# Kernel optimization log

Hardware: AMD Instinct MI355X
Metric: run time of the kernel (lower is better)

## Reference

```python
import jax, jax.numpy as jnp
import numpy as np

B, L, Z, G = 512, 2713, 58, 8  # batch, chem features, seq len (zeta), d_model (gamma)
H, HD, FF, NL = 8, 1, 2048, 6  # heads, head_dim, ffn dim, layers
RNA_IN, LIN1, LIN2 = 1018, 256, 64
CAT, C1, C2 = LIN2 + Z * G, 64, 8  # 528, 64, 8


def setup_inputs() -> dict:
    key = jax.random.key(0)
    ks = iter(jax.random.split(key, 40))
    r = lambda shape, s=0.05: (jax.random.normal(next(ks), shape, dtype=jnp.float32) * s)
    inp = {
        'rna': jax.random.normal(next(ks), (B, RNA_IN), dtype=jnp.float32),
        'drug': jax.random.normal(next(ks), (B, L, Z), dtype=jnp.float32),
        'lin1_w': r((LIN1, RNA_IN)), 'lin1_b': r((LIN1,)),
        'lin2_w': r((LIN2, LIN1)), 'lin2_b': r((LIN2,)),
        'chem_w': r((G, L)),  # chem_embedding: Linear(2713->8, no bias)
        'pos_w': r((G, Z)),   # pos_embedding on one-hot == its weight columns
        'qkv_w': r((NL, 3 * G, G)), 'qkv_b': r((NL, 3 * G)),
        'out_w': r((NL, G, G)), 'out_b': r((NL, G)),
        'ln1_g': jnp.ones((NL, G), jnp.float32), 'ln1_b': jnp.zeros((NL, G), jnp.float32),
        'ff1_w': r((NL, FF, G)), 'ff1_b': r((NL, FF)),
        'ff2_w': r((NL, G, FF)), 'ff2_b': r((NL, G)),
        'ln2_g': jnp.ones((NL, G), jnp.float32), 'ln2_b': jnp.zeros((NL, G), jnp.float32),
        'c1_w': r((C1, CAT)), 'c1_b': r((C1,)),
        'c2_w': r((C2, C1)), 'c2_b': r((C2,)),
        'c3_w': r((1, C2)), 'c3_b': r((1,)),
    }
    return inp


def _layernorm(x, g, b, eps=1e-5):
    mu = jnp.mean(x, axis=-1, keepdims=True)
    var = jnp.mean(jnp.square(x - mu), axis=-1, keepdims=True)
    return (x - mu) * jax.lax.rsqrt(var + eps) * g + b


def _forward(rna, drug, lin1_w, lin1_b, lin2_w, lin2_b, chem_w, pos_w,
             qkv_w, qkv_b, out_w, out_b, ln1_g, ln1_b,
             ff1_w, ff1_b, ff2_w, ff2_b, ln2_g, ln2_b,
             c1_w, c1_b, c2_w, c2_b, c3_w, c3_b):
    # rna branch: two linear layers (no activation in original forward)
    r = rna @ lin1_w.T + lin1_b
    r = r @ lin2_w.T + lin2_b  # [B, 64]

    # Embedding: E = W_chem @ M + W_pos (the double loop, vectorized)
    E = jnp.einsum('gl,blz->bgz', chem_w, drug) + pos_w[None]  # [B, G, Z]
    x = jnp.transpose(E, (0, 2, 1))  # [B, Z, G] (batch_first transformer input)

    scale = 1.0 / np.sqrt(HD)
    for i in range(NL):  # 6 post-norm TransformerEncoderLayers, relu FFN
        qkv = x @ qkv_w[i].T + qkv_b[i]  # [B, Z, 3G]
        q, k, v = jnp.split(qkv, 3, axis=-1)
        qh = q.reshape(B, Z, H, HD)
        kh = k.reshape(B, Z, H, HD)
        vh = v.reshape(B, Z, H, HD)
        scores = jnp.einsum('bshd,bthd->bhst', qh, kh) * scale
        a = jax.nn.softmax(scores, axis=-1)
        o = jnp.einsum('bhst,bthd->bshd', a, vh).reshape(B, Z, G)
        o = o @ out_w[i].T + out_b[i]
        x = _layernorm(x + o, ln1_g[i], ln1_b[i])
        ff = jax.nn.relu(x @ ff1_w[i].T + ff1_b[i]) @ ff2_w[i].T + ff2_b[i]
        x = _layernorm(x + ff, ln2_g[i], ln2_b[i])

    flat = x.reshape(B, Z * G)  # [B, 464]
    h = jnp.concatenate([r, flat], axis=1)  # [B, 528]
    h = h @ c1_w.T + c1_b
    h = h @ c2_w.T + c2_b
    return h @ c3_w.T + c3_b  # [B, 1]


def reference(rna, drug, lin1_w, lin1_b, lin2_w, lin2_b, chem_w, pos_w,
              qkv_w, qkv_b, out_w, out_b, ln1_g, ln1_b,
              ff1_w, ff1_b, ff2_w, ff2_b, ln2_g, ln2_b,
              c1_w, c1_b, c2_w, c2_b, c3_w, c3_b):
    return _forward(rna, drug, lin1_w, lin1_b, lin2_w, lin2_b, chem_w, pos_w,
                    qkv_w, qkv_b, out_w, out_b, ln1_g, ln1_b,
                    ff1_w, ff1_b, ff2_w, ff2_b, ln2_g, ln2_b,
                    c1_w, c1_b, c2_w, c2_b, c3_w, c3_b)
```

## Files before the change

kernel.cpp:

```cpp
#include <hip/hip_runtime.h>

#define BB 512
#define LDIM 2713
#define ZDIM 58
#define GDIM 8
#define NLAYER 6
#define FFDIM 2048
#define RNAIN 1018
#define CATDIM 528
#define NCAT 1482
#define LQ 679

typedef float v2f __attribute__((ext_vector_type(2)));
typedef float f32x4 __attribute__((ext_vector_type(4)));
typedef _Float16 f16x4 __attribute__((ext_vector_type(4)));

#define OFF_TMATT  0
#define OFF_BR     16384
#define OFF_WCATT  16448
#define OFF_BPRIME 111296
#define OFF_W1H    111360
#define OFF_A2H    160512
#define OFF_EPART  209664

__global__ __launch_bounds__(512, 8) void embed_kernel(
    const float* __restrict__ drug, const float* __restrict__ chem_w,
    float* __restrict__ epart) {
    __shared__ float cwl[LQ * 8 + 8];
    __shared__ float part[8][ZDIM][8];
    const int bq = blockIdx.x;
    const int b = bq >> 2, q = bq & 3;
    const int t = threadIdx.x;
    const int w = t >> 6;
    const int lane = t & 63;
    const int l0 = q * LQ;
    const int nrows = (LDIM - l0 < LQ) ? (LDIM - l0) : LQ;

    #pragma unroll
    for (int g = 0; g < 8; ++g)
        for (int i = t; i < nrows; i += 512)
            cwl[i * 8 + g] = chem_w[g * LDIM + l0 + i];
    __syncthreads();

    {
        int z = (lane < ZDIM) ? lane : (ZDIM - 1);
        const float* dp = drug + (size_t)b * (LDIM * ZDIM) + (size_t)l0 * ZDIM;
        v2f a0 = {0.f, 0.f}, a1 = {0.f, 0.f}, a2 = {0.f, 0.f}, a3 = {0.f, 0.f};
        int r0 = w * 85;
        int r1 = (r0 + 85 < nrows) ? (r0 + 85) : nrows;
        int r = r0;
        for (; r + 4 <= r1; r += 4) {
            float d0 = dp[(r + 0) * ZDIM + z];
            float d1 = dp[(r + 1) * ZDIM + z];
            float d2 = dp[(r + 2) * ZDIM + z];
            float d3 = dp[(r + 3) * ZDIM + z];
            const v2f* c0 = (const v2f*)(cwl + (r + 0) * 8);
            const v2f* c1 = (const v2f*)(cwl + (r + 1) * 8);
            const v2f* c2 = (const v2f*)(cwl + (r + 2) * 8);
            const v2f* c3 = (const v2f*)(cwl + (r + 3) * 8);
            v2f dd;
            dd = (v2f){d0, d0};
            a0 += c0[0] * dd; a1 += c0[1] * dd; a2 += c0[2] * dd; a3 += c0[3] * dd;
            dd = (v2f){d1, d1};
            a0 += c1[0] * dd; a1 += c1[1] * dd; a2 += c1[2] * dd; a3 += c1[3] * dd;
            dd = (v2f){d2, d2};
            a0 += c2[0] * dd; a1 += c2[1] * dd; a2 += c2[2] * dd; a3 += c2[3] * dd;
            dd = (v2f){d3, d3};
            a0 += c3[0] * dd; a1 += c3[1] * dd; a2 += c3[2] * dd; a3 += c3[3] * dd;
        }
        for (; r < r1; ++r) {
            float d = dp[r * ZDIM + z];
            const v2f* cc = (const v2f*)(cwl + r * 8);
            v2f dd = {d, d};
            a0 += cc[0] * dd; a1 += cc[1] * dd; a2 += cc[2] * dd; a3 += cc[3] * dd;
        }
        if (lane < ZDIM) {
            v2f* pr = (v2f*)(&part[w][z][0]);
            pr[0] = a0; pr[1] = a1; pr[2] = a2; pr[3] = a3;
        }
    }
    __syncthreads();
    if (t < 464) {
        int z = t >> 3, g = t & 7;
        float s = 0.f;
        #pragma unroll
        for (int ww = 0; ww < 8; ++ww) s += part[ww][z][g];
        epart[(size_t)bq * 464 + t] = s;
    }
}

__global__ void prep0_kernel(const float* __restrict__ ff1_w, const float* __restrict__ ff2_w,
                             const float* __restrict__ c1_w, const float* __restrict__ lin2_w,
                             const float* __restrict__ lin1_b, const float* __restrict__ lin2_b,
                             float* __restrict__ ws) {
    int tid = blockIdx.x * 256 + threadIdx.x;
    float* TmatT = ws + OFF_TMATT;
    float* bR    = ws + OFF_BR;
    _Float16* w1hp = (_Float16*)(ws + OFF_W1H);
    _Float16* a2hp = (_Float16*)(ws + OFF_A2H);

    int r1 = tid;
    if (r1 < NLAYER * 128 * 32) {
        int li = r1 / 4096, rem = r1 % 4096;
        int ft = rem >> 5, l32 = rem & 31;
        int q = l32 >> 4, i = l32 & 15;
        const float* src = ff1_w + ((size_t)li * FFDIM + ft * 16 + i) * 8 + q * 4;
        size_t dst = ((size_t)(li * 128 + ft) * 32 + l32) * 4;
        #pragma unroll
        for (int j = 0; j < 4; ++j) w1hp[dst + j] = (_Float16)src[j];
        return;
    }
    int r2 = r1 - NLAYER * 128 * 32;
    if (r2 < NLAYER * 128 * 32) {
        int li = r2 / 4096, rem = r2 % 4096;
        int ft = rem >> 5, s = rem & 31;
        int q = s >> 3, i2 = s & 7;
        const float* src = ff2_w + ((size_t)li * GDIM + i2) * FFDIM + ft * 16 + q * 4;
        size_t dst = ((size_t)(li * 128 + ft) * 32 + s) * 4;
        #pragma unroll
        for (int j = 0; j < 4; ++j) a2hp[dst + j] = (_Float16)src[j];
        return;
    }
    int r3 = r2 - NLAYER * 128 * 32;
    if (r3 < 256 * 64) {
        int n = r3 >> 6, j = r3 & 63;
        float a = 0.f;
        for (int m = 0; m < 64; ++m) a += c1_w[j * CATDIM + m] * lin2_w[m * 256 + n];
        TmatT[r3] = a;
        return;
    }
    int r4 = r3 - 256 * 64;
    if (r4 < 64) {
        float a = lin2_b[r4];
        for (int n = 0; n < 256; ++n) a += lin2_w[r4 * 256 + n] * lin1_b[n];
        bR[r4] = a;
    }
}

__global__ void prep1_kernel(const float* __restrict__ lin1_w, const float* __restrict__ c1_w,
                             const float* __restrict__ c1_b, float* __restrict__ ws) {
    int tid = blockIdx.x * 256 + threadIdx.x;
    const float* TmatT = ws + OFF_TMATT;
    const float* bR    = ws + OFF_BR;
    float* WcatT  = ws + OFF_WCATT;
    float* bprime = ws + OFF_BPRIME;
    if (tid < RNAIN * 64) {
        int k = tid >> 6, j = tid & 63;
        float a = 0.f;
        #pragma unroll 4
        for (int n = 0; n < 256; ++n) a += TmatT[n * 64 + j] * lin1_w[n * RNAIN + k];
        WcatT[tid] = a;
        return;
    }
    int q = tid - RNAIN * 64;
    if (q < 464 * 64) {
        int kk = q >> 6, j = q & 63;
        WcatT[(RNAIN + kk) * 64 + j] = c1_w[j * CATDIM + 64 + kk];
        return;
    }
    int j = q - 464 * 64;
    if (j < 64) {
        float a = c1_b[j];
        for (int m = 0; m < 64; ++m) a += c1_w[j * CATDIM + m] * bR[m];
        bprime[j] = a;
    }
}

__global__ __launch_bounds__(1024, 8) void main_kernel(
    const float* __restrict__ epart, const float* __restrict__ pos_w,
    const _Float16* __restrict__ w1h, const _Float16* __restrict__ a2h,
    const float* __restrict__ ff1_b,
    const float* __restrict__ qkv_w, const float* __restrict__ qkv_b,
    const float* __restrict__ out_w, const float* __restrict__ out_b,
    const float* __restrict__ ln1_g, const float* __restrict__ ln1_b,
    const float* __restrict__ ff2_b,
    const float* __restrict__ ln2_g, const float* __restrict__ ln2_b,
    const float* __restrict__ rna, const float* __restrict__ WcatT,
    const float* __restrict__ bprime,
    const float* __restrict__ c2_w, const float* __restrict__ c2_b,
    const float* __restrict__ c3_w, const float* __restrict__ c3_b,
    float* __restrict__ out) {
    __shared__ float smem[12712];
    float* xs    = smem;
    float* qs    = smem + 512;
    float* ks    = smem + 992;
    float* vs    = smem + 1472;
    float* os    = smem + 1952;
    float* part  = smem + 2464;
    float* qkvws = smem + 10656;
    float* qkvbs = smem + 11808;
    float* outws = smem + 11952;
    float* outbs = smem + 12336;
    float* l1gs  = smem + 12384;
    float* l1bs  = smem + 12432;
    float* l2gs  = smem + 12480;
    float* l2bs  = smem + 12528;
    float* f2bs  = smem + 12576;
    float* h1s   = smem + 12624;
    float* h2s   = smem + 12688;

    const int b = blockIdx.x;
    const int t = threadIdx.x;
    const int w = __builtin_amdgcn_readfirstlane(t >> 6);
    const int lane = t & 63;
    const int quad = lane >> 4;
    const int i16 = lane & 15;

    for (int i = t; i < 1152; i += 1024) qkvws[i] = qkv_w[i];
    if (t < 144) qkvbs[t] = qkv_b[t];
    if (t < 384) outws[t] = out_w[t];
    if (t < 48) {
        outbs[t] = out_b[t];
        l1gs[t] = ln1_g[t]; l1bs[t] = ln1_b[t];
        l2gs[t] = ln2_g[t]; l2bs[t] = ln2_b[t];
        f2bs[t] = ff2_b[t];
    }

    if (t < 512) {
        if (t < 464) {
            int z = t >> 3, g = t & 7;
            const float* ep = epart + (size_t)(b * 4) * 464 + t;
            float s = ep[0] + ep[464] + ep[928] + ep[1392] + pos_w[g * ZDIM + z];
            xs[t] = s;
        } else {
            xs[t] = 0.f;
        }
    }
    __syncthreads();

    for (int li = 0; li < NLAYER; ++li) {
        if (t < 464) {
            int z = t >> 3, h = t & 7;
            const float4* xr = (const float4*)(xs + z * 8);
            float4 x0 = xr[0], x1 = xr[1];
            #pragma unroll
            for (int p = 0; p < 3; ++p) {
                int j = p * 8 + h;
                const float4* wr = (const float4*)(qkvws + li * 192 + j * 8);
                float4 w0 = wr[0], w1 = wr[1];
                float a = qkvbs[li * 24 + j]
                        + x0.x * w0.x + x0.y * w0.y + x0.z * w0.z + x0.w * w0.w
                        + x1.x * w1.x + x1.y * w1.y + x1.z * w1.z + x1.w * w1.w;
                float* dst = (p == 0) ? qs : (p == 1) ? ks : vs;
                dst[h * 60 + z] = a;
            }
        }
        __syncthreads();

        if (t < 464) {
            int h = t & 7, s = t >> 3;
            float q = qs[h * 60 + s];
            const float4* kr = (const float4*)(ks + h * 60);
            const float4* vr = (const float4*)(vs + h * 60);
            float sum = 0.f, oa = 0.f;
            #pragma unroll 2
            for (int c = 0; c < 14; ++c) {
                float4 k4 = kr[c], v4 = vr[c];
                float e0 = __expf(q * k4.x); sum += e0; oa += e0 * v4.x;
                float e1 = __expf(q * k4.y); sum += e1; oa += e1 * v4.y;
                float e2 = __expf(q * k4.z); sum += e2; oa += e2 * v4.z;
                float e3 = __expf(q * k4.w); sum += e3; oa += e3 * v4.w;
            }
            {
                const float* kk = ks + h * 60;
                const float* vv = vs + h * 60;
                float e0 = __expf(q * kk[56]); sum += e0; oa += e0 * vv[56];
                float e1 = __expf(q * kk[57]); sum += e1; oa += e1 * vv[57];
            }
            os[t] = oa / sum;
        }
        __syncthreads();

        if (t < 464) {
            int z = t >> 3, g = t & 7;
            const float4* orow = (const float4*)(os + z * 8);
            float4 o0 = orow[0], o1 = orow[1];
            const float4* wr = (const float4*)(outws + li * 64 + g * 8);
            float4 w0 = wr[0], w1 = wr[1];
            float a = outbs[li * 8 + g] + xs[t]
                    + o0.x * w0.x + o0.y * w0.y + o0.z * w0.z + o0.w * w0.w
                    + o1.x * w1.x + o1.y * w1.y + o1.z * w1.z + o1.w * w1.w;
            float s8 = a + __shfl_xor(a, 1);
            s8 += __shfl_xor(s8, 2);
            s8 += __shfl_xor(s8, 4);
            float mu = s8 * 0.125f;
            float d = a - mu;
            float vv = d * d;
            vv += __shfl_xor(vv, 1); vv += __shfl_xor(vv, 2); vv += __shfl_xor(vv, 4);
            float inv = rsqrtf(vv * 0.125f + 1e-5f);
            xs[t] = d * inv * l1gs[li * 8 + g] + l1bs[li * 8 + g];
        }
        __syncthreads();

        {
            f16x4 xb[4];
            #pragma unroll
            for (int nt = 0; nt < 4; ++nt) {
                if (quad < 2) {
                    const float4* xp = (const float4*)(xs + (nt * 16 + i16) * 8 + quad * 4);
                    float4 xv = *xp;
                    xb[nt][0] = (_Float16)xv.x; xb[nt][1] = (_Float16)xv.y;
                    xb[nt][2] = (_Float16)xv.z; xb[nt][3] = (_Float16)xv.w;
                } else {
                    xb[nt][0] = (_Float16)0.f; xb[nt][1] = (_Float16)0.f;
                    xb[nt][2] = (_Float16)0.f; xb[nt][3] = (_Float16)0.f;
                }
            }
            f32x4 oacc[4];
            #pragma unroll
            for (int nt = 0; nt < 4; ++nt) { oacc[nt][0]=0.f; oacc[nt][1]=0.f; oacc[nt][2]=0.f; oacc[nt][3]=0.f; }

            const _Float16* w1p = w1h + ((size_t)(li * 128 + w * 8) * 32) * 4;
            const _Float16* a2p = a2h + ((size_t)(li * 128 + w * 8) * 32) * 4;
            const float* b1p = ff1_b + li * FFDIM + w * 128;

            #pragma unroll 2
            for (int ft = 0; ft < 8; ++ft) {
                f16x4 w1f = {};
                if (lane < 32) w1f = *(const f16x4*)(w1p + (size_t)(ft * 32 + lane) * 4);
                f16x4 a2f = {};
                if (i16 < 8) a2f = *(const f16x4*)(a2p + (size_t)(ft * 32 + quad * 8 + i16) * 4);
                f32x4 b1v = *(const f32x4*)(b1p + ft * 16 + quad * 4);
                #pragma unroll
                for (int nt = 0; nt < 4; ++nt) {
                    f32x4 h = b1v;
                    h = __builtin_amdgcn_mfma_f32_16x16x16f16(w1f, xb[nt], h, 0, 0, 0);
                    h[0] = fmaxf(h[0], 0.f); h[1] = fmaxf(h[1], 0.f);
                    h[2] = fmaxf(h[2], 0.f); h[3] = fmaxf(h[3], 0.f);
                    f16x4 hb;
                    hb[0] = (_Float16)h[0]; hb[1] = (_Float16)h[1];
                    hb[2] = (_Float16)h[2]; hb[3] = (_Float16)h[3];
                    oacc[nt] = __builtin_amdgcn_mfma_f32_16x16x16f16(a2f, hb, oacc[nt], 0, 0, 0);
                }
            }
            if (quad < 2) {
                #pragma unroll
                for (int nt = 0; nt < 4; ++nt) {
                    float4 o4 = make_float4(oacc[nt][0], oacc[nt][1], oacc[nt][2], oacc[nt][3]);
                    *(float4*)(part + ((w * 64 + nt * 16 + i16) * 8 + quad * 4)) = o4;
                }
            }
        }
        __syncthreads();

        if (t < 464) {
            int z = t >> 3, g = t & 7;
            float s = 0.f;
            #pragma unroll
            for (int ww = 0; ww < 16; ++ww) s += part[(ww * 64 + z) * 8 + g];
            float a = xs[t] + s + f2bs[li * 8 + g];
            float s8 = a + __shfl_xor(a, 1);
            s8 += __shfl_xor(s8, 2);
            s8 += __shfl_xor(s8, 4);
            float mu = s8 * 0.125f;
            float d = a - mu;
            float vv = d * d;
            vv += __shfl_xor(vv, 1); vv += __shfl_xor(vv, 2); vv += __shfl_xor(vv, 4);
            float inv = rsqrtf(vv * 0.125f + 1e-5f);
            xs[t] = d * inv * l2gs[li * 8 + g] + l2bs[li * 8 + g];
        }
        __syncthreads();
    }

    {
        float* cat = part;
        float* partial = part + 4096;
        const float* rg = rna + (size_t)b * RNAIN;
        for (int i = t; i < RNAIN; i += 1024) cat[i] = rg[i];
        __syncthreads();
        int j = lane;
        int k0 = w * 93;
        int k1 = (k0 + 93 < NCAT) ? (k0 + 93) : NCAT;
        float a = (w == 0) ? bprime[j] : 0.f;
        #pragma unroll 4
        for (int k = k0; k < k1; ++k) {
            float ck = (k < RNAIN) ? cat[k] : xs[k - RNAIN];
            a += ck * WcatT[k * 64 + j];
        }
        partial[w * 64 + j] = a;
        __syncthreads();
        if (t < 64) {
            float s = 0.f;
            #pragma unroll
            for (int ww = 0; ww < 16; ++ww) s += partial[ww * 64 + t];
            h1s[t] = s;
        }
    }
    __syncthreads();
    if (t < 8) {
        float a2 = c2_b[t];
        #pragma unroll 8
        for (int m = 0; m < 64; ++m) a2 += h1s[m] * c2_w[t * 64 + m];
        h2s[t] = a2;
    }
    __syncthreads();
    if (t == 0) {
        float a3 = c3_b[0];
        #pragma unroll
        for (int jj = 0; jj < 8; ++jj) a3 += h2s[jj] * c3_w[jj];
        out[b] = a3;
    }
}

extern "C" void kernel_launch(void* const* d_in, const int* in_sizes, int n_in,
                              void* d_out, int out_size, void* d_ws, size_t ws_size,
                              hipStream_t stream) {
    const float* rna    = (const float*)d_in[0];
    const float* drug   = (const float*)d_in[1];
    const float* lin1_w = (const float*)d_in[2];
    const float* lin1_b = (const float*)d_in[3];
    const float* lin2_w = (const float*)d_in[4];
    const float* lin2_b = (const float*)d_in[5];
    const float* chem_w = (const float*)d_in[6];
    const float* pos_w  = (const float*)d_in[7];
    const float* qkv_w  = (const float*)d_in[8];
    const float* qkv_b  = (const float*)d_in[9];
    const float* out_w  = (const float*)d_in[10];
    const float* out_b  = (const float*)d_in[11];
    const float* ln1_g  = (const float*)d_in[12];
    const float* ln1_b  = (const float*)d_in[13];
    const float* ff1_w  = (const float*)d_in[14];
    const float* ff1_b  = (const float*)d_in[15];
    const float* ff2_w  = (const float*)d_in[16];
    const float* ff2_b  = (const float*)d_in[17];
    const float* ln2_g  = (const float*)d_in[18];
    const float* ln2_b  = (const float*)d_in[19];
    const float* c1_w   = (const float*)d_in[20];
    const float* c1_b   = (const float*)d_in[21];
    const float* c2_w   = (const float*)d_in[22];
    const float* c2_b   = (const float*)d_in[23];
    const float* c3_w   = (const float*)d_in[24];
    const float* c3_b   = (const float*)d_in[25];
    float* ws  = (float*)d_ws;
    float* out = (float*)d_out;

    float* epart          = ws + OFF_EPART;
    const _Float16* w1h   = (const _Float16*)(ws + OFF_W1H);
    const _Float16* a2h   = (const _Float16*)(ws + OFF_A2H);
    const float* WcatT    = ws + OFF_WCATT;
    const float* bprime   = ws + OFF_BPRIME;

    hipLaunchKernelGGL(embed_kernel, dim3(BB * 4), dim3(512), 0, stream,
                       drug, chem_w, epart);
    hipLaunchKernelGGL(prep0_kernel, dim3(257), dim3(256), 0, stream,
                       ff1_w, ff2_w, c1_w, lin2_w, lin1_b, lin2_b, ws);
    hipLaunchKernelGGL(prep1_kernel, dim3(371), dim3(256), 0, stream,
                       lin1_w, c1_w, c1_b, ws);
    hipLaunchKernelGGL(main_kernel, dim3(BB), dim3(1024), 0, stream,
                       epart, pos_w, w1h, a2h, ff1_b,
                       qkv_w, qkv_b, out_w, out_b,
                       ln1_g, ln1_b, ff2_b, ln2_g, ln2_b,
                       rna, WcatT, bprime, c2_w, c2_b, c3_w, c3_b, out);
}
```

Baseline: 610.7 us.

## Fuse embedding into main kernel and merge prep kernels, drop fp16 weight repack

Moves the chem embedding reduction into the main per-batch kernel, so each 1024-thread block streams its own drug slice in four chunks and skips the epart round trip through global memory. The two prep kernels become one 17-block kernel that keeps the intermediate c1·lin2 product in shared memory. The FFN weights are now read as fp32 from the original layout and converted to fp16 in registers, which removes the repack pass but doubles weight bytes per load and adds conversion work. The embedding now runs on only 512 blocks instead of 2048, so it has less parallelism for the memory-bound drug read, and each prep block recomputes the 256x64 product.

Result: slower. 732.6 us (+20.0%).

```diff
diff --git a/kernel.cpp b/kernel.cpp
--- a/kernel.cpp
+++ b/kernel.cpp
@@ -15,160 +15,63 @@
 typedef float f32x4 __attribute__((ext_vector_type(4)));
 typedef _Float16 f16x4 __attribute__((ext_vector_type(4)));
 
-#define OFF_TMATT  0
-#define OFF_BR     16384
-#define OFF_WCATT  16448
-#define OFF_BPRIME 111296
-#define OFF_W1H    111360
-#define OFF_A2H    160512
-#define OFF_EPART  209664
-
-__global__ __launch_bounds__(512, 8) void embed_kernel(
+#define OFF_WCATT  0
+#define OFF_BPRIME 94848
+
+__global__ __launch_bounds__(1024) void prep_kernel(
+    const float* __restrict__ lin1_w, const float* __restrict__ lin1_b,
+    const float* __restrict__ lin2_w, const float* __restrict__ lin2_b,
+    const float* __restrict__ c1_w, const float* __restrict__ c1_b,
+    float* __restrict__ ws) {
+    __shared__ float Tm[16384];
+    const int t = threadIdx.x;
+    float* WcatT = ws + OFF_WCATT;
+
+    if (blockIdx.x == 16) {
+        if (t < 64) {
+            float a = lin2_b[t];
+            #pragma unroll 4
+            for (int n = 0; n < 256; ++n) a += lin2_w[t * 256 + n] * lin1_b[n];
+            Tm[t] = a;
+        }
+        __syncthreads();
+        if (t < 64) {
+            float a = c1_b[t];
+            #pragma unroll 4
+            for (int m = 0; m < 64; ++m) a += c1_w[t * CATDIM + m] * Tm[m];
+            ws[OFF_BPRIME + t] = a;
+        }
+        for (int i = t; i < 464 * 64; i += 1024) {
+            int kk = i >> 6, j = i & 63;
+            WcatT[(RNAIN + kk) * 64 + j] = c1_w[j * CATDIM + 64 + kk];
+        }
+        return;
+    }
+
+    for (int i = t; i < 16384; i += 1024) {
+        int n = i >> 6, j = i & 63;
+        float a = 0.f;
+        #pragma unroll 8
+        for (int m = 0; m < 64; ++m) a += c1_w[j * CATDIM + m] * lin2_w[m * 256 + n];
+        Tm[i] = a;
+    }
+    __syncthreads();
+    const int k0 = blockIdx.x * 64;
+    const int j = t & 63;
+    for (int kr = t >> 6; kr < 64; kr += 16) {
+        int k = k0 + kr;
+        if (k >= RNAIN) break;
+        float a = 0.f;
+        #pragma unroll 8
+        for (int n = 0; n < 256; ++n) a += Tm[n * 64 + j] * lin1_w[n * RNAIN + k];
+        WcatT[k * 64 + j] = a;
+    }
+}
+
+__global__ __launch_bounds__(1024, 8) void mega_kernel(
     const float* __restrict__ drug, const float* __restrict__ chem_w,
-    float* __restrict__ epart) {
-    __shared__ float cwl[LQ * 8 + 8];
-    __shared__ float part[8][ZDIM][8];
-    const int bq = blockIdx.x;
-    const int b = bq >> 2, q = bq & 3;
-    const int t = threadIdx.x;
-    const int w = t >> 6;
-    const int lane = t & 63;
-    const int l0 = q * LQ;
-    const int nrows = (LDIM - l0 < LQ) ? (LDIM - l0) : LQ;
-
-    #pragma unroll
-    for (int g = 0; g < 8; ++g)
-        for (int i = t; i < nrows; i += 512)
-            cwl[i * 8 + g] = chem_w[g * LDIM + l0 + i];
-    __syncthreads();
-
-    {
-        int z = (lane < ZDIM) ? lane : (ZDIM - 1);
-        const float* dp = drug + (size_t)b * (LDIM * ZDIM) + (size_t)l0 * ZDIM;
-        v2f a0 = {0.f, 0.f}, a1 = {0.f, 0.f}, a2 = {0.f, 0.f}, a3 = {0.f, 0.f};
-        int r0 = w * 85;
-        int r1 = (r0 + 85 < nrows) ? (r0 + 85) : nrows;
-        int r = r0;
-        for (; r + 4 <= r1; r += 4) {
-            float d0 = dp[(r + 0) * ZDIM + z];
-            float d1 = dp[(r + 1) * ZDIM + z];
-            float d2 = dp[(r + 2) * ZDIM + z];
-            float d3 = dp[(r + 3) * ZDIM + z];
-            const v2f* c0 = (const v2f*)(cwl + (r + 0) * 8);
-            const v2f* c1 = (const v2f*)(cwl + (r + 1) * 8);
-            const v2f* c2 = (const v2f*)(cwl + (r + 2) * 8);
-            const v2f* c3 = (const v2f*)(cwl + (r + 3) * 8);
-            v2f dd;
-            dd = (v2f){d0, d0};
-            a0 += c0[0] * dd; a1 += c0[1] * dd; a2 += c0[2] * dd; a3 += c0[3] * dd;
-            dd = (v2f){d1, d1};
-            a0 += c1[0] * dd; a1 += c1[1] * dd; a2 += c1[2] * dd; a3 += c1[3] * dd;
-            dd = (v2f){d2, d2};
-            a0 += c2[0] * dd; a1 += c2[1] * dd; a2 += c2[2] * dd; a3 += c2[3] * dd;
-            dd = (v2f){d3, d3};
-            a0 += c3[0] * dd; a1 += c3[1] * dd; a2 += c3[2] * dd; a3 += c3[3] * dd;
-        }
-        for (; r < r1; ++r) {
-            float d = dp[r * ZDIM + z];
-            const v2f* cc = (const v2f*)(cwl + r * 8);
-            v2f dd = {d, d};
-            a0 += cc[0] * dd; a1 += cc[1] * dd; a2 += cc[2] * dd; a3 += cc[3] * dd;
-        }
-        if (lane < ZDIM) {
-            v2f* pr = (v2f*)(&part[w][z][0]);
-            pr[0] = a0; pr[1] = a1; pr[2] = a2; pr[3] = a3;
-        }
-    }
-    __syncthreads();
-    if (t < 464) {
-        int z = t >> 3, g = t & 7;
-        float s = 0.f;
-        #pragma unroll
-        for (int ww = 0; ww < 8; ++ww) s += part[ww][z][g];
-        epart[(size_t)bq * 464 + t] = s;
-    }
-}
-
-__global__ void prep0_kernel(const float* __restrict__ ff1_w, const float* __restrict__ ff2_w,
-                             const float* __restrict__ c1_w, const float* __restrict__ lin2_w,
-                             const float* __restrict__ lin1_b, const float* __restrict__ lin2_b,
-                             float* __restrict__ ws) {
-    int tid = blockIdx.x * 256 + threadIdx.x;
-    float* TmatT = ws + OFF_TMATT;
-    float* bR    = ws + OFF_BR;
-    _Float16* w1hp = (_Float16*)(ws + OFF_W1H);
-    _Float16* a2hp = (_Float16*)(ws + OFF_A2H);
-
-    int r1 = tid;
-    if (r1 < NLAYER * 128 * 32) {
-        int li = r1 / 4096, rem = r1 % 4096;
-        int ft = rem >> 5, l32 = rem & 31;
-        int q = l32 >> 4, i = l32 & 15;
-        const float* src = ff1_w + ((size_t)li * FFDIM + ft * 16 + i) * 8 + q * 4;
-        size_t dst = ((size_t)(li * 128 + ft) * 32 + l32) * 4;
-        #pragma unroll
-        for (int j = 0; j < 4; ++j) w1hp[dst + j] = (_Float16)src[j];
-        return;
-    }
-    int r2 = r1 - NLAYER * 128 * 32;
-    if (r2 < NLAYER * 128 * 32) {
-        int li = r2 / 4096, rem = r2 % 4096;
-        int ft = rem >> 5, s = rem & 31;
-        int q = s >> 3, i2 = s & 7;
-        const float* src = ff2_w + ((size_t)li * GDIM + i2) * FFDIM + ft * 16 + q * 4;
-        size_t dst = ((size_t)(li * 128 + ft) * 32 + s) * 4;
-        #pragma unroll
-        for (int j = 0; j < 4; ++j) a2hp[dst + j] = (_Float16)src[j];
-        return;
-    }
-    int r3 = r2 - NLAYER * 128 * 32;
-    if (r3 < 256 * 64) {
-        int n = r3 >> 6, j = r3 & 63;
-        float a = 0.f;
-        for (int m = 0; m < 64; ++m) a += c1_w[j * CATDIM + m] * lin2_w[m * 256 + n];
-        TmatT[r3] = a;
-        return;
-    }
-    int r4 = r3 - 256 * 64;
-    if (r4 < 64) {
-        float a = lin2_b[r4];
-        for (int n = 0; n < 256; ++n) a += lin2_w[r4 * 256 + n] * lin1_b[n];
-        bR[r4] = a;
-    }
-}
-
-__global__ void prep1_kernel(const float* __restrict__ lin1_w, const float* __restrict__ c1_w,
-                             const float* __restrict__ c1_b, float* __restrict__ ws) {
-    int tid = blockIdx.x * 256 + threadIdx.x;
-    const float* TmatT = ws + OFF_TMATT;
-    const float* bR    = ws + OFF_BR;
-    float* WcatT  = ws + OFF_WCATT;
-    float* bprime = ws + OFF_BPRIME;
-    if (tid < RNAIN * 64) {
-        int k = tid >> 6, j = tid & 63;
-        float a = 0.f;
-        #pragma unroll 4
-        for (int n = 0; n < 256; ++n) a += TmatT[n * 64 + j] * lin1_w[n * RNAIN + k];
-        WcatT[tid] = a;
-        return;
-    }
-    int q = tid - RNAIN * 64;
-    if (q < 464 * 64) {
-        int kk = q >> 6, j = q & 63;
-        WcatT[(RNAIN + kk) * 64 + j] = c1_w[j * CATDIM + 64 + kk];
-        return;
-    }
-    int j = q - 464 * 64;
-    if (j < 64) {
-        float a = c1_b[j];
-        for (int m = 0; m < 64; ++m) a += c1_w[j * CATDIM + m] * bR[m];
-        bprime[j] = a;
-    }
-}
-
-__global__ __launch_bounds__(1024, 8) void main_kernel(
-    const float* __restrict__ epart, const float* __restrict__ pos_w,
-    const _Float16* __restrict__ w1h, const _Float16* __restrict__ a2h,
+    const float* __restrict__ pos_w,
+    const float* __restrict__ ff1_w, const float* __restrict__ ff2_w,
     const float* __restrict__ ff1_b,
     const float* __restrict__ qkv_w, const float* __restrict__ qkv_b,
     const float* __restrict__ out_w, const float* __restrict__ out_b,
@@ -180,7 +83,9 @@
     const float* __restrict__ c2_w, const float* __restrict__ c2_b,
     const float* __restrict__ c3_w, const float* __restrict__ c3_b,
     float* __restrict__ out) {
-    __shared__ float smem[12712];
+    __shared__ float smem[12864];
+    float* cwl    = smem;
+    float* part_e = smem + 5440;
     float* xs    = smem;
     float* qs    = smem + 512;
     float* ks    = smem + 992;
@@ -206,6 +111,67 @@
     const int quad = lane >> 4;
     const int i16 = lane & 15;
 
+    {
+        const int zc = (lane < ZDIM) ? lane : (ZDIM - 1);
+        v2f acc0 = {0.f, 0.f}, acc1 = {0.f, 0.f}, acc2 = {0.f, 0.f}, acc3 = {0.f, 0.f};
+        for (int q = 0; q < 4; ++q) {
+            const int l0 = q * LQ;
+            const int nrows = (LDIM - l0 < LQ) ? (LDIM - l0) : LQ;
+            __syncthreads();
+            #pragma unroll
+            for (int g = 0; g < 8; ++g)
+                for (int i = t; i < nrows; i += 1024)
+                    cwl[i * 8 + g] = chem_w[g * LDIM + l0 + i];
+            __syncthreads();
+            const float* dp = drug + (size_t)b * (LDIM * ZDIM) + (size_t)l0 * ZDIM;
+            int r0 = w * 43;
+            int r1 = (r0 + 43 < nrows) ? (r0 + 43) : nrows;
+            int r = r0;
+            for (; r + 4 <= r1; r += 4) {
+                float d0 = dp[(r + 0) * ZDIM + zc];
+                float d1 = dp[(r + 1) * ZDIM + zc];
+                float d2 = dp[(r + 2) * ZDIM + zc];
+                float d3 = dp[(r + 3) * ZDIM + zc];
+                const v2f* c0 = (const v2f*)(cwl + (r + 0) * 8);
+                const v2f* c1 = (const v2f*)(cwl + (r + 1) * 8);
+                const v2f* c2 = (const v2f*)(cwl + (r + 2) * 8);
+                const v2f* c3 = (const v2f*)(cwl + (r + 3) * 8);
+                v2f dd;
+                dd = (v2f){d0, d0};
+                acc0 += c0[0] * dd; acc1 += c0[1] * dd; acc2 += c0[2] * dd; acc3 += c0[3] * dd;
+                dd = (v2f){d1, d1};
+                acc0 += c1[0] * dd; acc1 += c1[1] * dd; acc2 += c1[2] * dd; acc3 += c1[3] * dd;
+                dd = (v2f){d2, d2};
+                acc0 += c2[0] * dd; acc1 += c2[1] * dd; acc2 += c2[2] * dd; acc3 += c2[3] * dd;
+                dd = (v2f){d3, d3};
+                acc0 += c3[0] * dd; acc1 += c3[1] * dd; acc2 += c3[2] * dd; acc3 += c3[3] * dd;
+            }
+            for (; r < r1; ++r) {
+                float d = dp[r * ZDIM + zc];
+                const v2f* cc = (const v2f*)(cwl + r * 8);
+                v2f dd = {d, d};
+                acc0 += cc[0] * dd; acc1 += cc[1] * dd; acc2 += cc[2] * dd; acc3 += cc[3] * dd;
+            }
+        }
+        if (lane < ZDIM) {
+            v2f* pr = (v2f*)(part_e + w * 464 + zc * 8);
+            pr[0] = acc0; pr[1] = acc1; pr[2] = acc2; pr[3] = acc3;
+        }
+        __syncthreads();
+        if (t < 512) {
+            if (t < 464) {
+                int z = t >> 3, g = t & 7;
+                float s = pos_w[g * ZDIM + z];
+                #pragma unroll
+                for (int ww = 0; ww < 16; ++ww) s += part_e[ww * 464 + t];
+                xs[t] = s;
+            } else {
+                xs[t] = 0.f;
+            }
+        }
+        __syncthreads();
+    }
+
     for (int i = t; i < 1152; i += 1024) qkvws[i] = qkv_w[i];
     if (t < 144) qkvbs[t] = qkv_b[t];
     if (t < 384) outws[t] = out_w[t];
@@ -214,17 +180,6 @@
         l1gs[t] = ln1_g[t]; l1bs[t] = ln1_b[t];
         l2gs[t] = ln2_g[t]; l2bs[t] = ln2_b[t];
         f2bs[t] = ff2_b[t];
-    }
-
-    if (t < 512) {
-        if (t < 464) {
-            int z = t >> 3, g = t & 7;
-            const float* ep = epart + (size_t)(b * 4) * 464 + t;
-            float s = ep[0] + ep[464] + ep[928] + ep[1392] + pos_w[g * ZDIM + z];
-            xs[t] = s;
-        } else {
-            xs[t] = 0.f;
-        }
     }
     __syncthreads();
 
@@ -310,16 +265,24 @@
             #pragma unroll
             for (int nt = 0; nt < 4; ++nt) { oacc[nt][0]=0.f; oacc[nt][1]=0.f; oacc[nt][2]=0.f; oacc[nt][3]=0.f; }
 
-            const _Float16* w1p = w1h + ((size_t)(li * 128 + w * 8) * 32) * 4;
-            const _Float16* a2p = a2h + ((size_t)(li * 128 + w * 8) * 32) * 4;
+            const float* w1p = ff1_w + ((size_t)li * FFDIM + w * 128) * 8;
+            const float* a2p = ff2_w + (size_t)li * GDIM * FFDIM + w * 128;
             const float* b1p = ff1_b + li * FFDIM + w * 128;
 
             #pragma unroll 2
             for (int ft = 0; ft < 8; ++ft) {
                 f16x4 w1f = {};
-                if (lane < 32) w1f = *(const f16x4*)(w1p + (size_t)(ft * 32 + lane) * 4);
+                if (lane < 32) {
+                    f32x4 v = *(const f32x4*)(w1p + (size_t)(ft * 16 + i16) * 8 + quad * 4);
+                    w1f[0] = (_Float16)v[0]; w1f[1] = (_Float16)v[1];
+                    w1f[2] = (_Float16)v[2]; w1f[3] = (_Float16)v[3];
+                }
                 f16x4 a2f = {};
-                if (i16 < 8) a2f = *(const f16x4*)(a2p + (size_t)(ft * 32 + quad * 8 + i16) * 4);
+                if (i16 < 8) {
+                    f32x4 v = *(const f32x4*)(a2p + (size_t)i16 * FFDIM + ft * 16 + quad * 4);
+                    a2f[0] = (_Float16)v[0]; a2f[1] = (_Float16)v[1];
+                    a2f[2] = (_Float16)v[2]; a2f[3] = (_Float16)v[3];
+                }
                 f32x4 b1v = *(const f32x4*)(b1p + ft * 16 + quad * 4);
                 #pragma unroll
                 for (int nt = 0; nt < 4; ++nt) {
@@ -434,21 +397,12 @@
     float* ws  = (float*)d_ws;
     float* out = (float*)d_out;
 
-    float* epart          = ws + OFF_EPART;
-    const _Float16* w1h   = (const _Float16*)(ws + OFF_W1H);
-    const _Float16* a2h   = (const _Float16*)(ws + OFF_A2H);
-    const float* WcatT    = ws + OFF_WCATT;
-    const float* bprime   = ws + OFF_BPRIME;
-
-    hipLaunchKernelGGL(embed_kernel, dim3(BB * 4), dim3(512), 0, stream,
-                       drug, chem_w, epart);
-    hipLaunchKernelGGL(prep0_kernel, dim3(257), dim3(256), 0, stream,
-                       ff1_w, ff2_w, c1_w, lin2_w, lin1_b, lin2_b, ws);
-    hipLaunchKernelGGL(prep1_kernel, dim3(371), dim3(256), 0, stream,
-                       lin1_w, c1_w, c1_b, ws);
-    hipLaunchKernelGGL(main_kernel, dim3(BB), dim3(1024), 0, stream,
-                       epart, pos_w, w1h, a2h, ff1_b,
+    hipLaunchKernelGGL(prep_kernel, dim3(17), dim3(1024), 0, stream,
+                       lin1_w, lin1_b, lin2_w, lin2_b, c1_w, c1_b, ws);
+    hipLaunchKernelGGL(mega_kernel, dim3(BB), dim3(1024), 0, stream,
+                       drug, chem_w, pos_w, ff1_w, ff2_w, ff1_b,
                        qkv_w, qkv_b, out_w, out_b,
                        ln1_g, ln1_b, ff2_b, ln2_g, ln2_b,
-                       rna, WcatT, bprime, c2_w, c2_b, c3_w, c3_b, out);
+                       rna, ws + OFF_WCATT, ws + OFF_BPRIME,
+                       c2_w, c2_b, c3_w, c3_b, out);
 }
```
